# Performance work log

Hardware: AMD Instinct MI355X
Metric: run time of the kernel (lower is better)

Reference implementation:

```python
import jax, jax.numpy as jnp
import numpy as np
from jax import lax

# Module hyperparameters (init_kwargs)
B, T, F, H = 512, 256, 64, 128
D = F + H            # decoder LSTMCell width = input_dim + hidden_rnn
OUT_DIM = 32         # output_dim (survival horizon steps)
RISKS = 2
NEG = -1e10


def lstm_cell(x, h, c, Wih, Whh):
    # PyTorch gate order: i, f, g, o; bias=False
    g = x @ Wih.T + h @ Whh.T
    i, f, gg, o = jnp.split(g, 4, axis=-1)
    c = jax.nn.sigmoid(f) * c + jax.nn.sigmoid(i) * jnp.tanh(gg)
    h = jax.nn.sigmoid(o) * jnp.tanh(c)
    return h, c


def setup_inputs() -> dict:
    key = jax.random.key(0)
    ks = jax.random.split(key, 12)
    rn = lambda k, shp, fan: jax.random.normal(k, shp, jnp.float32) * (1.0 / np.sqrt(fan))
    return {
        "x": jax.random.normal(ks[0], (B, T, F), jnp.float32),
        # encoder LSTM (1 layer, bias=False)
        "W_ih_emb": rn(ks[1], (4 * H, F), F),
        "W_hh_emb": rn(ks[2], (4 * H, H), H),
        # longitudinal head: Linear(H -> F)
        "W_long": rn(ks[3], (F, H), H),
        "b_long": jnp.zeros((F,), jnp.float32),
        # attention head: Linear(F+H -> 1)
        "W_att": rn(ks[4], (1, D), D),
        "b_att": jnp.zeros((1,), jnp.float32),
        # per-risk cause-specific LSTMCell (bias=False) and Linear(D -> 1)
        "W_ih_cs": rn(ks[5], (RISKS, 4 * D, D), D),
        "W_hh_cs": rn(ks[6], (RISKS, 4 * D, D), D),
        "W_cs": rn(ks[7], (RISKS, 1, D), D),
        "b_cs": jnp.zeros((RISKS, 1), jnp.float32),
    }


def _forward(x, W_ih_emb, W_hh_emb, W_long, b_long, W_att, b_att,
             W_ih_cs, W_hh_cs, W_cs, b_cs):
    inputmask = jnp.abs(x).sum(2) == 0                      # [B,T]
    last_obs = (~inputmask).sum(axis=1) - 1                 # [B]

    # encoder LSTM over time
    def enc_step(carry, xt):
        h, c = carry
        h, c = lstm_cell(xt, h, c, W_ih_emb, W_hh_emb)
        return (h, c), h

    h0 = jnp.zeros((x.shape[0], H), x.dtype)
    _, hs = lax.scan(enc_step, (h0, h0), x.transpose(1, 0, 2))
    hidden = hs.transpose(1, 0, 2)                          # [B,T,H]

    long_pred = hidden @ W_long.T + b_long                  # [B,T,F]

    x_last = x[jnp.arange(x.shape[0]), last_obs]            # [B,F]
    concat = jnp.concatenate(
        [hidden, jnp.broadcast_to(x_last[:, None, :], (x.shape[0], x.shape[1], F))], -1)
    scores = (concat @ W_att.T + b_att)[..., 0]             # [B,T]

    idx = jnp.arange(x.shape[1])[None, :]
    scores = jnp.where(idx >= last_obs[:, None], NEG, scores)
    att = jax.nn.softmax(scores, axis=1)
    att = jnp.where((last_obs > 0)[:, None], att, 0.0)      # rows with last_obs==0 zeroed

    hidden_att = jnp.einsum('bt,bth->bh', att, hidden)      # [B,H]
    ha = jnp.concatenate([hidden_att, x_last], 1)           # [B,D]

    state0 = (lax.stop_gradient(ha), lax.stop_gradient(ha))  # .detach() on init state
    rs = jnp.arange(OUT_DIM * RISKS) % RISKS                # k-major, r-minor loop order

    def dec_step(carry, r):
        h, c = carry
        h, c = lstm_cell(ha, h, c, W_ih_cs[r], W_hh_cs[r])
        out = jax.nn.sigmoid(h @ W_cs[r].T + b_cs[r])       # [B,1]
        return (h, c), out

    _, outs = lax.scan(dec_step, state0, rs)                # [steps,B,1]
    outcomes = jax.nn.softmax(outs[..., 0].T, axis=-1)      # [B, OUT_DIM*RISKS]
    parts = tuple(outcomes[:, i * OUT_DIM:(i + 1) * OUT_DIM] for i in range(RISKS))
    return (long_pred,) + parts


def reference(x, W_ih_emb, W_hh_emb, W_long, b_long, W_att, b_att,
              W_ih_cs, W_hh_cs, W_cs, b_cs):
    return _forward(x, W_ih_emb, W_hh_emb, W_long, b_long, W_att, b_att,
                    W_ih_cs, W_hh_cs, W_cs, b_cs)
```

## Files before the change

### kernel.cpp

```cpp
#include <hip/hip_runtime.h>
#include <stdint.h>

#define DEV __device__ __forceinline__
typedef unsigned short u16; typedef unsigned int u32; typedef unsigned long long u64;
typedef __attribute__((ext_vector_type(8))) short s8v;
typedef __attribute__((ext_vector_type(4))) float f4v;

#define Bb 512
#define Tt 256
#define Ff 64
#define Hh 128
#define Dd 192
#define L2E  1.4426950408889634f
#define L2E2 2.8853900817779268f

DEV u16 f2bf(float f){ u32 u = __builtin_bit_cast(u32, f); u32 r = (u + 0x7fffu + ((u>>16)&1u)) >> 16; return (u16)r; }
DEV float bf2f(u16 h){ u32 u = ((u32)h)<<16; return __builtin_bit_cast(float, u); }
DEV float sigm(float x){ return __builtin_amdgcn_rcpf(1.0f + __expf(-x)); }
DEV float ex2(float x){ float r; asm("v_exp_f32 %0, %1" : "=v"(r) : "v"(x)); return r; }
DEV float sig2n(float y){ return __builtin_amdgcn_rcpf(1.0f + ex2(y)); }
DEV float th2 (float y){ return 1.0f - 2.0f*__builtin_amdgcn_rcpf(1.0f + ex2(y)); }
DEV u32 cvtpk(float lo, float hi){ u32 d; asm("v_cvt_pk_bf16_f32 %0, %1, %2" : "=v"(d) : "v"(lo), "v"(hi)); return d; }

DEV f4v mfma16(s8v a, s8v b, f4v c){ return __builtin_amdgcn_mfma_f32_16x16x32_bf16(a, b, c, 0, 0, 0); }

DEV void barrier_lds(){ asm volatile("s_waitcnt lgkmcnt(0)\n\ts_barrier" ::: "memory"); }

DEV int hxe(int k, int c){ int blk = k>>3; return (blk*16 + (c ^ ((blk&3)<<1)))*8 + (k&7); }

DEV s8v pack8s(const float* p, float sc){
  const float4 a = *(const float4*)p; const float4 b = *(const float4*)(p+4);
  s8v r; r[0]=(short)f2bf(a.x*sc); r[1]=(short)f2bf(a.y*sc); r[2]=(short)f2bf(a.z*sc); r[3]=(short)f2bf(a.w*sc);
  r[4]=(short)f2bf(b.x*sc); r[5]=(short)f2bf(b.y*sc); r[6]=(short)f2bf(b.z*sc); r[7]=(short)f2bf(b.w*sc); return r;
}
DEV s8v pack8(const float* p){ return pack8s(p, 1.0f); }
DEV u32 pk2(float a, float b){ return (u32)f2bf(a) | ((u32)f2bf(b)<<16); }

__global__ __launch_bounds__(64) void prelim_k(const float* __restrict__ x,
    const float* __restrict__ Watt, const float* __restrict__ batt,
    float* __restrict__ xlast, float* __restrict__ c0, int* __restrict__ lastobs)
{
  int b = blockIdx.x, tid = threadIdx.x;
  int cnt = 0;
  for (int it = 0; it < 4; ++it){
    int t = it*64 + tid;
    const float4* p = (const float4*)(x + ((size_t)b*Tt + t)*Ff);
    float s = 0.0f;
    #pragma unroll
    for (int q = 0; q < 16; ++q){ float4 v = p[q]; s += fabsf(v.x)+fabsf(v.y)+fabsf(v.z)+fabsf(v.w); }
    u64 m = __ballot(s != 0.0f);
    cnt += __popcll(m);
  }
  int last = cnt - 1;
  int li = (last < 0) ? (Tt-1) : last;
  float xl = x[((size_t)b*Tt + li)*Ff + tid];
  xlast[b*Ff + tid] = xl;
  float p = xl * Watt[Hh + tid];
  for (int off = 32; off; off >>= 1) p += __shfl_down(p, off);
  if (tid == 0){ c0[b] = p + batt[0]; lastobs[b] = last; }
}

__global__ __launch_bounds__(256) void prep_wd_k(const float* __restrict__ Whhcs,
    const float* __restrict__ Wihcs, u16* __restrict__ Wd, u16* __restrict__ WdIH)
{
  int idx = blockIdx.x*256 + threadIdx.x;
  int j = idx & 7, lane = (idx>>3)&63;
  int f = idx>>9;
  int kt = f % 6; int mtr = f/6;
  int mt = mtr % 48, r = mtr/48;
  int ut = mt>>2, g = mt&3;
  int row = g*Dd + ut*16 + (lane&15);
  int k = kt*32 + (lane>>4)*8 + j;
  float sc = (g == 2) ? L2E2 : -L2E;
  size_t src = ((size_t)r*768 + row)*Dd + k;
  Wd[idx]   = f2bf(Whhcs[src] * sc);
  WdIH[idx] = f2bf(Wihcs[src] * sc);
}

__global__ __launch_bounds__(64) void xw_k(const u16* __restrict__ WdIH,
    const float* __restrict__ ha, u16* __restrict__ xwg)
{
  int lane = threadIdx.x, l15 = lane&15, l4 = lane>>4;
  int cg = blockIdx.x & 3, rm = blockIdx.x >> 2;
  s8v af[6];
  #pragma unroll
  for (int kt=0;kt<6;++kt) af[kt] = *(const s8v*)(WdIH + (size_t)(rm*6+kt)*512 + lane*8);
  #pragma unroll
  for (int ct=0; ct<8; ++ct){
    int c = cg*128 + ct*16 + l15;
    f4v a = {0,0,0,0};
    #pragma unroll
    for (int kt=0;kt<6;++kt){
      s8v b = pack8(ha + (size_t)c*Dd + kt*32 + l4*8);
      a = mfma16(af[kt], b, a);
    }
    int bg = cg*8 + ct;
    int base = bg*24576 + rm*256 + l15*16 + l4*4;
    *(u32*)&xwg[base]   = pk2(a[0], a[1]);
    *(u32*)&xwg[base+2] = pk2(a[2], a[3]);
  }
}

__global__ __launch_bounds__(512)
__attribute__((amdgpu_waves_per_eu(2,2)))
void enc_k(
    const float* __restrict__ x, const float* __restrict__ Whh, const float* __restrict__ Wih,
    const float* __restrict__ Wlong, const float* __restrict__ blong, const float* __restrict__ Watt,
    const float* __restrict__ xlast, const float* __restrict__ c0v, const int* __restrict__ lastobs,
    float* __restrict__ lp_out, float* __restrict__ ha)
{
  __shared__ __align__(16) u16 hx[2][3072];
  __shared__ float sarr[2][16];
  const int tid = threadIdx.x, wid = tid>>6, lane = tid&63, l15 = lane&15, l4 = lane>>4;
  const int b0 = blockIdx.x*16;
  const int xrow = tid>>5, xc2 = (tid&31)*2;

  s8v wf[4][6];
  #pragma unroll
  for (int mt = 0; mt < 4; ++mt){
    int gate = mt*Hh + wid*16 + l15;
    float sc = (mt == 2) ? L2E2 : -L2E;
    #pragma unroll
    for (int kt = 0; kt < 6; ++kt){
      int k0 = kt*32 + l4*8;
      if (kt < 4) wf[mt][kt] = pack8s(Whh + (size_t)gate*Hh + k0, sc);
      else        wf[mt][kt] = pack8s(Wih + (size_t)gate*Ff + (k0 - Hh), sc);
    }
  }
  s8v wfx[6];
  {
    s8v z = {0,0,0,0,0,0,0,0};
    #pragma unroll
    for (int kt = 0; kt < 6; ++kt) wfx[kt] = z;
    if (wid < 4){
      int f = wid*16 + l15;
      #pragma unroll
      for (int kt = 0; kt < 4; ++kt) wfx[kt] = pack8(Wlong + (size_t)f*Hh + kt*32 + l4*8);
    } else if (wid == 4 && l15 == 0){
      #pragma unroll
      for (int kt = 0; kt < 4; ++kt) wfx[kt] = pack8(Watt + kt*32 + l4*8);
    }
  }
  float bl[4] = {0,0,0,0};
  if (wid < 4){
    #pragma unroll
    for (int j = 0; j < 4; ++j) bl[j] = blong[wid*16 + l4*4 + j];
  }
  const int   lastb = lastobs[b0 + l15];
  const float c0b   = c0v[b0 + l15];

  const int he0 = hxe(wid*16 + l4*4, l15);
  const int xe0 = hxe(Hh + xc2, xrow);
  float* lpb = lp_out + ((size_t)(b0+l15)*Tt)*Ff + wid*16 + l4*4;

  ((u64*)hx[0])[tid] = 0ull;
  {
    float2 xv = *(const float2*)(x + ((size_t)(b0+xrow)*Tt + 0)*Ff + xc2);
    *(u32*)&hx[0][xe0] = cvtpk(xv.x, xv.y);
  }
  float2 xa = *(const float2*)(x + ((size_t)(b0+xrow)*Tt + 1)*Ff + xc2);
  float2 xb;
  __syncthreads();

  float cst[4] = {0,0,0,0}, hp[4] = {0,0,0,0}, hpp[4] = {0,0,0,0};
  float accA[4] = {0,0,0,0}, mrun = -3.0e38f, zrun = 0.0f;

#define ENC_STEP(T_, CURB_, NXTB_, XC_, XN_) { \
    const int t = (T_); \
    s8v bf[6]; \
    _Pragma("unroll") \
    for (int kt = 0; kt < 6; ++kt) \
      bf[kt] = *(const s8v*)&hx[CURB_][((kt*4 + l4)*16 + (l15 ^ (l4<<1)))*8]; \
    { int tp = t + 2; if (tp > Tt-1) tp = Tt-1; \
      XN_ = *(const float2*)(x + ((size_t)(b0+xrow)*Tt + tp)*Ff + xc2); } \
    f4v acc0 = {0,0,0,0}, acc1 = {0,0,0,0}, acc2 = {0,0,0,0}, acc3 = {0,0,0,0}, accx = {0,0,0,0}; \
    _Pragma("unroll") \
    for (int kt = 0; kt < 6; ++kt){ \
      acc0 = mfma16(wf[0][kt], bf[kt], acc0); \
      acc1 = mfma16(wf[1][kt], bf[kt], acc1); \
      acc2 = mfma16(wf[2][kt], bf[kt], acc2); \
      acc3 = mfma16(wf[3][kt], bf[kt], acc3); \
    } \
    if (wid < 5){ \
      _Pragma("unroll") \
      for (int kt = 0; kt < 6; ++kt) accx = mfma16(wfx[kt], bf[kt], accx); \
    } \
    if (wid == 4 && l4 == 0) sarr[NXTB_][l15] = accx[0] + c0b; \
    float hnew[4]; \
    _Pragma("unroll") \
    for (int j = 0; j < 4; ++j){ \
      float si = sig2n(acc0[j]), sf = sig2n(acc1[j]); \
      float tg = th2(acc2[j]),   so = sig2n(acc3[j]); \
      float cn = sf*cst[j] + si*tg; \
      cst[j] = cn; \
      hnew[j] = so * th2(cn * L2E2); \
    } \
    if (t >= 2){ \
      float sv = sarr[CURB_][l15]; \
      if (t-2 < lastb){ \
        float mn = fmaxf(mrun, sv); \
        float sc = __expf(mrun - mn); \
        float e  = __expf(sv - mn); \
        zrun = zrun*sc + e; \
        _Pragma("unroll") \
        for (int j = 0; j < 4; ++j) accA[j] = accA[j]*sc + e*hpp[j]; \
        mrun = mn; \
      } \
    } \
    _Pragma("unroll") \
    for (int j = 0; j < 4; ++j){ hpp[j] = hp[j]; hp[j] = hnew[j]; } \
    { u32 plo = cvtpk(hnew[0], hnew[1]), phi = cvtpk(hnew[2], hnew[3]); \
      *(u64*)&hx[NXTB_][he0] = (u64)plo | ((u64)phi<<32); } \
    if (t < Tt-1) *(u32*)&hx[NXTB_][xe0] = cvtpk(XC_.x, XC_.y); \
    if (wid < 4 && t >= 1){ \
      float4 v; v.x = accx[0]+bl[0]; v.y = accx[1]+bl[1]; v.z = accx[2]+bl[2]; v.w = accx[3]+bl[3]; \
      *(float4*)(lpb + (size_t)(t-1)*Ff) = v; \
    } \
    barrier_lds(); }

  for (int tp2 = 0; tp2 < 128; ++tp2){
    ENC_STEP(2*tp2,   0, 1, xa, xb)
    ENC_STEP(2*tp2+1, 1, 0, xb, xa)
  }
#undef ENC_STEP

  {
    if (254 < lastb){
      float sv = sarr[0][l15];
      float mn = fmaxf(mrun, sv);
      float sc = __expf(mrun - mn);
      float e  = __expf(sv - mn);
      zrun = zrun*sc + e;
      #pragma unroll
      for (int j = 0; j < 4; ++j) accA[j] = accA[j]*sc + e*hpp[j];
      mrun = mn;
    }
    s8v bfE[4];
    #pragma unroll
    for (int kt = 0; kt < 4; ++kt)
      bfE[kt] = *(const s8v*)&hx[0][((kt*4 + l4)*16 + (l15 ^ (l4<<1)))*8];
    if (wid < 4){
      f4v accx = {0,0,0,0};
      #pragma unroll
      for (int kt = 0; kt < 4; ++kt) accx = mfma16(wfx[kt], bfE[kt], accx);
      float4 v; v.x = accx[0]+bl[0]; v.y = accx[1]+bl[1]; v.z = accx[2]+bl[2]; v.w = accx[3]+bl[3];
      *(float4*)(lpb + (size_t)(Tt-1)*Ff) = v;
    }
    float inv = (zrun > 0.0f) ? __builtin_amdgcn_rcpf(zrun) : 0.0f;
    #pragma unroll
    for (int j = 0; j < 4; ++j)
      ha[(size_t)(b0 + l15)*Dd + wid*16 + l4*4 + j] = accA[j]*inv;
    __syncthreads();
    for (int q = tid; q < 16*Ff; q += 512){
      int r2 = q >> 6, f = q & 63;
      ha[(size_t)(b0 + r2)*Dd + Hh + f] = xlast[(b0 + r2)*Ff + f];
    }
  }
}

__global__ __launch_bounds__(256)
__attribute__((amdgpu_waves_per_eu(1,1)))
void dec_k(const float* __restrict__ ha,
    const u16* __restrict__ Wd, const u16* __restrict__ xwg,
    const float* __restrict__ Wcs, const float* __restrict__ bcs, float* __restrict__ outs)
{
  __shared__ __align__(16) u16 hx[2][3072];
  __shared__ __align__(16) u16 w1[48*2*512];
  __shared__ __align__(16) u16 xwl[2*48*256];
  __shared__ float red[2][4][16];
  const int tid = threadIdx.x, wid = tid>>6, lane = tid&63, l15 = lane&15, l4 = lane>>4;
  const int b0 = blockIdx.x*16;

  #pragma unroll
  for (int it = 0; it < 3; ++it){
    int k = it*64 + (tid>>4)*4, c = tid&15;
    float4 v = *(const float4*)(ha + (size_t)(b0+c)*Dd + k);
    int e = hxe(k, c);
    *(u32*)&hx[0][e]   = cvtpk(v.x, v.y);
    *(u32*)&hx[0][e+2] = cvtpk(v.z, v.w);
  }
  {
    const u16* src = xwg + (size_t)blockIdx.x*24576;
    #pragma unroll
    for (int i = 0; i < 12; ++i){
      int off = (i*256 + tid)*8;
      *(s8v*)&xwl[off] = *(const s8v*)(src + off);
    }
  }
  #pragma unroll
  for (int i = 0; i < 24; ++i){
    int off = (i*256 + tid)*8;
    int chunk = off>>9, inner = off&511;
    int mtg = chunk>>1, kt = chunk&1;
    *(s8v*)&w1[off] = *(const s8v*)(Wd + (size_t)((48+mtg)*6+kt)*512 + inner);
  }
  s8v wreg[12][6];
  #pragma unroll
  for (int m = 0; m < 12; ++m)
    #pragma unroll
    for (int kt = 0; kt < 6; ++kt)
      wreg[m][kt] = *(const s8v*)(Wd + (size_t)((wid*12+m)*6+kt)*512 + lane*8);

  float cst[3][4], wcsr0[3][4], wcsr1[3][4];
  #pragma unroll
  for (int ut = 0; ut < 3; ++ut){
    int u0 = (wid*3+ut)*16 + l4*4;
    #pragma unroll
    for (int jj = 0; jj < 4; ++jj){
      cst[ut][jj]   = ha[(size_t)(b0+l15)*Dd + u0 + jj];
      wcsr0[ut][jj] = Wcs[u0 + jj];
      wcsr1[ut][jj] = Wcs[Dd + u0 + jj];
    }
  }
  const float bc0 = bcs[0], bc1 = bcs[1];
  __syncthreads();

  const u16* wsb = Wd + (size_t)(48 + wid*12)*6*512 + lane*8;
  s8v st[4][4];
#define LOADS_UT(ut_) { \
    _Pragma("unroll") for (int g_=0; g_<4; ++g_) \
      _Pragma("unroll") for (int q_=0; q_<4; ++q_) \
        st[g_][q_] = *(const s8v*)(wsb + (size_t)(((ut_)*4+g_)*6 + 2 + q_)*512); }

#define XWINIT(r_, m_, a_) { \
    int xb_ = ((r_)*48 + wid*12 + (m_))*256 + l15*16 + l4*4; \
    u64 q_ = *(const u64*)&xwl[xb_]; \
    u32 qlo_ = (u32)q_, qhi_ = (u32)(q_>>32); \
    a_[0] = __builtin_bit_cast(float, qlo_<<16); \
    a_[1] = __builtin_bit_cast(float, qlo_ & 0xffff0000u); \
    a_[2] = __builtin_bit_cast(float, qhi_<<16); \
    a_[3] = __builtin_bit_cast(float, qhi_ & 0xffff0000u); }

#define CELLS(ut_, wcs_, nxtb_, a0_, a1_, a2_, a3_) { \
    float hn[4]; \
    _Pragma("unroll") for (int j = 0; j < 4; ++j){ \
      float si = sig2n(a0_[j]), sf = sig2n(a1_[j]); \
      float tg = th2(a2_[j]),   so = sig2n(a3_[j]); \
      float cn = sf*cst[ut_][j] + si*tg; \
      cst[ut_][j] = cn; \
      hn[j] = so * th2(cn * L2E2); \
      part += hn[j] * wcs_[ut_][j]; } \
    u32 plo_ = cvtpk(hn[0], hn[1]), phi_ = cvtpk(hn[2], hn[3]); \
    int u0_ = (wid*3+(ut_))*16 + l4*4; \
    int e0_ = (((u0_>>3)*16) + (l15 ^ (((u0_>>3)&3)<<1)))*8 + (u0_&7); \
    *(u64*)&hx[nxtb_][e0_] = (u64)plo_ | ((u64)phi_<<32); }

  for (int sp = 0; sp < 32; ++sp){
    {
      s8v bf[6];
      #pragma unroll
      for (int kt = 0; kt < 6; ++kt)
        bf[kt] = *(const s8v*)&hx[0][((kt*4 + l4)*16 + (l15 ^ (l4<<1)))*8];
      LOADS_UT(0);
      float part = 0.0f;
      #pragma unroll
      for (int ut = 0; ut < 3; ++ut){
        f4v a0,a1,a2,a3;
        XWINIT(0, ut*4+0, a0); XWINIT(0, ut*4+1, a1); XWINIT(0, ut*4+2, a2); XWINIT(0, ut*4+3, a3);
        #pragma unroll
        for (int kt = 0; kt < 6; ++kt){
          a0 = mfma16(wreg[ut*4+0][kt], bf[kt], a0);
          a1 = mfma16(wreg[ut*4+1][kt], bf[kt], a1);
          a2 = mfma16(wreg[ut*4+2][kt], bf[kt], a2);
          a3 = mfma16(wreg[ut*4+3][kt], bf[kt], a3);
        }
        CELLS(ut, wcsr0, 1, a0, a1, a2, a3);
      }
      part += __shfl_xor(part, 16); part += __shfl_xor(part, 32);
      if (l4 == 0) red[0][wid][l15] = part;
      barrier_lds();
      if (tid < 16)
        outs[(sp*2)*Bb + b0 + tid] = sigm(red[0][0][tid]+red[0][1][tid]+red[0][2][tid]+red[0][3][tid] + bc0);
    }
    {
      s8v bf[6];
      #pragma unroll
      for (int kt = 0; kt < 6; ++kt)
        bf[kt] = *(const s8v*)&hx[1][((kt*4 + l4)*16 + (l15 ^ (l4<<1)))*8];
      float part = 0.0f;
      #pragma unroll
      for (int ut = 0; ut < 3; ++ut){
        f4v a0,a1,a2,a3;
        XWINIT(1, ut*4+0, a0); XWINIT(1, ut*4+1, a1); XWINIT(1, ut*4+2, a2); XWINIT(1, ut*4+3, a3);
        #pragma unroll
        for (int kt = 0; kt < 2; ++kt){
          s8v q0 = *(const s8v*)&w1[((wid*12+ut*4+0)*2+kt)*512 + lane*8];
          s8v q1 = *(const s8v*)&w1[((wid*12+ut*4+1)*2+kt)*512 + lane*8];
          s8v q2 = *(const s8v*)&w1[((wid*12+ut*4+2)*2+kt)*512 + lane*8];
          s8v q3 = *(const s8v*)&w1[((wid*12+ut*4+3)*2+kt)*512 + lane*8];
          a0 = mfma16(q0, bf[kt], a0);
          a1 = mfma16(q1, bf[kt], a1);
          a2 = mfma16(q2, bf[kt], a2);
          a3 = mfma16(q3, bf[kt], a3);
        }
        #pragma unroll
        for (int q = 0; q < 4; ++q){
          a0 = mfma16(st[0][q], bf[2+q], a0);
          a1 = mfma16(st[1][q], bf[2+q], a1);
          a2 = mfma16(st[2][q], bf[2+q], a2);
          a3 = mfma16(st[3][q], bf[2+q], a3);
        }
        if (ut < 2) LOADS_UT(ut+1);
        CELLS(ut, wcsr1, 0, a0, a1, a2, a3);
      }
      part += __shfl_xor(part, 16); part += __shfl_xor(part, 32);
      if (l4 == 0) red[1][wid][l15] = part;
      barrier_lds();
      if (tid < 16)
        outs[(sp*2+1)*Bb + b0 + tid] = sigm(red[1][0][tid]+red[1][1][tid]+red[1][2][tid]+red[1][3][tid] + bc1);
    }
  }
#undef LOADS_UT
#undef XWINIT
#undef CELLS
}

__global__ __launch_bounds__(256) void fin_k(const float* __restrict__ outs, float* __restrict__ dout)
{
  int row = blockIdx.x*256 + threadIdx.x;
  float v[64]; float mx = -3.0e38f;
  #pragma unroll
  for (int s = 0; s < 64; ++s){ v[s] = outs[s*Bb + row]; mx = fmaxf(mx, v[s]); }
  float sum = 0.0f;
  #pragma unroll
  for (int s = 0; s < 64; ++s){ v[s] = __expf(v[s] - mx); sum += v[s]; }
  float inv = __builtin_amdgcn_rcpf(sum);
  float* p0 = dout + (size_t)Bb*Tt*Ff;
  float* p1 = p0 + Bb*32;
  #pragma unroll
  for (int j = 0; j < 32; ++j) p0[row*32 + j] = v[j]*inv;
  #pragma unroll
  for (int j = 0; j < 32; ++j) p1[row*32 + j] = v[32 + j]*inv;
}

extern "C" void kernel_launch(void* const* d_in, const int* in_sizes, int n_in,
                              void* d_out, int out_size, void* d_ws, size_t ws_size,
                              hipStream_t stream)
{
  const float* x      = (const float*)d_in[0];
  const float* Wih    = (const float*)d_in[1];
  const float* Whh    = (const float*)d_in[2];
  const float* Wlong  = (const float*)d_in[3];
  const float* blong  = (const float*)d_in[4];
  const float* Watt   = (const float*)d_in[5];
  const float* batt   = (const float*)d_in[6];
  const float* Wihcs  = (const float*)d_in[7];
  const float* Whhcs  = (const float*)d_in[8];
  const float* Wcs    = (const float*)d_in[9];
  const float* bcs    = (const float*)d_in[10];
  float* out = (float*)d_out;
  char* ws = (char*)d_ws;

  float* xlast   = (float*)ws;
  float* c0      = (float*)(ws + 131072);
  int*   lastobs = (int*)  (ws + 133120);
  float* ha      = (float*)(ws + 135168);
  u16*   Wd      = (u16*)  (ws + 528384);
  u16*   WdIH    = (u16*)  (ws + 1118208);
  u16*   xwg     = (u16*)  (ws + 1708032);
  float* outs    = (float*)(ws + 3280896);

  prep_wd_k<<<1152, 256, 0, stream>>>(Whhcs, Wihcs, Wd, WdIH);
  prelim_k<<<Bb, 64, 0, stream>>>(x, Watt, batt, xlast, c0, lastobs);
  enc_k<<<32, 512, 0, stream>>>(x, Whh, Wih, Wlong, blong, Watt, xlast, c0, lastobs, out, ha);
  xw_k<<<384, 64, 0, stream>>>(WdIH, ha, xwg);
  dec_k<<<32, 256, 0, stream>>>(ha, Wd, xwg, Wcs, bcs, outs);
  fin_k<<<2, 256, 0, stream>>>(outs, out);
}
```

Baseline: 544.1 us.

## Spread decoder across 12 waves with register-resident weights and unswizzled LDS layout

```diff
diff --git a/kernel.cpp b/kernel.cpp
--- a/kernel.cpp
+++ b/kernel.cpp
@@ -15,18 +15,19 @@
 #define L2E2 2.8853900817779268f
 
 DEV u16 f2bf(float f){ u32 u = __builtin_bit_cast(u32, f); u32 r = (u + 0x7fffu + ((u>>16)&1u)) >> 16; return (u16)r; }
-DEV float bf2f(u16 h){ u32 u = ((u32)h)<<16; return __builtin_bit_cast(float, u); }
 DEV float sigm(float x){ return __builtin_amdgcn_rcpf(1.0f + __expf(-x)); }
 DEV float ex2(float x){ float r; asm("v_exp_f32 %0, %1" : "=v"(r) : "v"(x)); return r; }
 DEV float sig2n(float y){ return __builtin_amdgcn_rcpf(1.0f + ex2(y)); }
 DEV float th2 (float y){ return 1.0f - 2.0f*__builtin_amdgcn_rcpf(1.0f + ex2(y)); }
 DEV u32 cvtpk(float lo, float hi){ u32 d; asm("v_cvt_pk_bf16_f32 %0, %1, %2" : "=v"(d) : "v"(lo), "v"(hi)); return d; }
+DEV float blo(u32 q){ return __builtin_bit_cast(float, q<<16); }
+DEV float bhi(u32 q){ return __builtin_bit_cast(float, q & 0xffff0000u); }
 
 DEV f4v mfma16(s8v a, s8v b, f4v c){ return __builtin_amdgcn_mfma_f32_16x16x32_bf16(a, b, c, 0, 0, 0); }
 
 DEV void barrier_lds(){ asm volatile("s_waitcnt lgkmcnt(0)\n\ts_barrier" ::: "memory"); }
 
-DEV int hxe(int k, int c){ int blk = k>>3; return (blk*16 + (c ^ ((blk&3)<<1)))*8 + (k&7); }
+DEV int hxe2(int k, int c){ return (k>>5)*512 + (((k>>3)&3)*16 + c)*8 + (k&7); }
 
 DEV s8v pack8s(const float* p, float sc){
   const float4 a = *(const float4*)p; const float4 b = *(const float4*)(p+4);
@@ -57,7 +58,7 @@
   xlast[b*Ff + tid] = xl;
   float p = xl * Watt[Hh + tid];
   for (int off = 32; off; off >>= 1) p += __shfl_down(p, off);
-  if (tid == 0){ c0[b] = p + batt[0]; lastobs[b] = last; }
+  if (tid == 0){ c0[b] = (p + batt[0]) * L2E; lastobs[b] = last; }
 }
 
 __global__ __launch_bounds__(256) void prep_wd_k(const float* __restrict__ Whhcs,
@@ -138,7 +139,7 @@
       for (int kt = 0; kt < 4; ++kt) wfx[kt] = pack8(Wlong + (size_t)f*Hh + kt*32 + l4*8);
     } else if (wid == 4 && l15 == 0){
       #pragma unroll
-      for (int kt = 0; kt < 4; ++kt) wfx[kt] = pack8(Watt + kt*32 + l4*8);
+      for (int kt = 0; kt < 4; ++kt) wfx[kt] = pack8s(Watt + kt*32 + l4*8, L2E);
     }
   }
   float bl[4] = {0,0,0,0};
@@ -149,8 +150,8 @@
   const int   lastb = lastobs[b0 + l15];
   const float c0b   = c0v[b0 + l15];
 
-  const int he0 = hxe(wid*16 + l4*4, l15);
-  const int xe0 = hxe(Hh + xc2, xrow);
+  const int he0 = hxe2(wid*16 + l4*4, l15);
+  const int xe0 = hxe2(Hh + xc2, xrow);
   float* lpb = lp_out + ((size_t)(b0+l15)*Tt)*Ff + wid*16 + l4*4;
 
   ((u64*)hx[0])[tid] = 0ull;
@@ -170,7 +171,7 @@
     s8v bf[6]; \
     _Pragma("unroll") \
     for (int kt = 0; kt < 6; ++kt) \
-      bf[kt] = *(const s8v*)&hx[CURB_][((kt*4 + l4)*16 + (l15 ^ (l4<<1)))*8]; \
+      bf[kt] = *(const s8v*)&hx[CURB_][kt*512 + lane*8]; \
     { int tp = t + 2; if (tp > Tt-1) tp = Tt-1; \
       XN_ = *(const float2*)(x + ((size_t)(b0+xrow)*Tt + tp)*Ff + xc2); } \
     f4v acc0 = {0,0,0,0}, acc1 = {0,0,0,0}, acc2 = {0,0,0,0}, acc3 = {0,0,0,0}, accx = {0,0,0,0}; \
@@ -199,8 +200,8 @@
       float sv = sarr[CURB_][l15]; \
       if (t-2 < lastb){ \
         float mn = fmaxf(mrun, sv); \
-        float sc = __expf(mrun - mn); \
-        float e  = __expf(sv - mn); \
+        float sc = ex2(mrun - mn); \
+        float e  = ex2(sv - mn); \
         zrun = zrun*sc + e; \
         _Pragma("unroll") \
         for (int j = 0; j < 4; ++j) accA[j] = accA[j]*sc + e*hpp[j]; \
@@ -228,8 +229,8 @@
     if (254 < lastb){
       float sv = sarr[0][l15];
       float mn = fmaxf(mrun, sv);
-      float sc = __expf(mrun - mn);
-      float e  = __expf(sv - mn);
+      float sc = ex2(mrun - mn);
+      float e  = ex2(sv - mn);
       zrun = zrun*sc + e;
       #pragma unroll
       for (int j = 0; j < 4; ++j) accA[j] = accA[j]*sc + e*hpp[j];
@@ -238,7 +239,7 @@
     s8v bfE[4];
     #pragma unroll
     for (int kt = 0; kt < 4; ++kt)
-      bfE[kt] = *(const s8v*)&hx[0][((kt*4 + l4)*16 + (l15 ^ (l4<<1)))*8];
+      bfE[kt] = *(const s8v*)&hx[0][kt*512 + lane*8];
     if (wid < 4){
       f4v accx = {0,0,0,0};
       #pragma unroll
@@ -258,161 +259,93 @@
   }
 }
 
-__global__ __launch_bounds__(256)
-__attribute__((amdgpu_waves_per_eu(1,1)))
+__global__ __launch_bounds__(768)
 void dec_k(const float* __restrict__ ha,
     const u16* __restrict__ Wd, const u16* __restrict__ xwg,
     const float* __restrict__ Wcs, const float* __restrict__ bcs, float* __restrict__ outs)
 {
   __shared__ __align__(16) u16 hx[2][3072];
-  __shared__ __align__(16) u16 w1[48*2*512];
-  __shared__ __align__(16) u16 xwl[2*48*256];
-  __shared__ float red[2][4][16];
+  __shared__ float red[2][12][16];
   const int tid = threadIdx.x, wid = tid>>6, lane = tid&63, l15 = lane&15, l4 = lane>>4;
   const int b0 = blockIdx.x*16;
 
-  #pragma unroll
-  for (int it = 0; it < 3; ++it){
-    int k = it*64 + (tid>>4)*4, c = tid&15;
+  {
+    int k = (tid>>4)*4, c = tid&15;
     float4 v = *(const float4*)(ha + (size_t)(b0+c)*Dd + k);
-    int e = hxe(k, c);
+    int e = hxe2(k, c);
     *(u32*)&hx[0][e]   = cvtpk(v.x, v.y);
     *(u32*)&hx[0][e+2] = cvtpk(v.z, v.w);
   }
-  {
-    const u16* src = xwg + (size_t)blockIdx.x*24576;
-    #pragma unroll
-    for (int i = 0; i < 12; ++i){
-      int off = (i*256 + tid)*8;
-      *(s8v*)&xwl[off] = *(const s8v*)(src + off);
-    }
-  }
-  #pragma unroll
-  for (int i = 0; i < 24; ++i){
-    int off = (i*256 + tid)*8;
-    int chunk = off>>9, inner = off&511;
-    int mtg = chunk>>1, kt = chunk&1;
-    *(s8v*)&w1[off] = *(const s8v*)(Wd + (size_t)((48+mtg)*6+kt)*512 + inner);
-  }
-  s8v wreg[12][6];
-  #pragma unroll
-  for (int m = 0; m < 12; ++m)
-    #pragma unroll
-    for (int kt = 0; kt < 6; ++kt)
-      wreg[m][kt] = *(const s8v*)(Wd + (size_t)((wid*12+m)*6+kt)*512 + lane*8);
-
-  float cst[3][4], wcsr0[3][4], wcsr1[3][4];
-  #pragma unroll
-  for (int ut = 0; ut < 3; ++ut){
-    int u0 = (wid*3+ut)*16 + l4*4;
-    #pragma unroll
-    for (int jj = 0; jj < 4; ++jj){
-      cst[ut][jj]   = ha[(size_t)(b0+l15)*Dd + u0 + jj];
-      wcsr0[ut][jj] = Wcs[u0 + jj];
-      wcsr1[ut][jj] = Wcs[Dd + u0 + jj];
-    }
-  }
-  const float bc0 = bcs[0], bc1 = bcs[1];
-  __syncthreads();
-
-  const u16* wsb = Wd + (size_t)(48 + wid*12)*6*512 + lane*8;
-  s8v st[4][4];
-#define LOADS_UT(ut_) { \
-    _Pragma("unroll") for (int g_=0; g_<4; ++g_) \
-      _Pragma("unroll") for (int q_=0; q_<4; ++q_) \
-        st[g_][q_] = *(const s8v*)(wsb + (size_t)(((ut_)*4+g_)*6 + 2 + q_)*512); }
-
-#define XWINIT(r_, m_, a_) { \
-    int xb_ = ((r_)*48 + wid*12 + (m_))*256 + l15*16 + l4*4; \
-    u64 q_ = *(const u64*)&xwl[xb_]; \
-    u32 qlo_ = (u32)q_, qhi_ = (u32)(q_>>32); \
-    a_[0] = __builtin_bit_cast(float, qlo_<<16); \
-    a_[1] = __builtin_bit_cast(float, qlo_ & 0xffff0000u); \
-    a_[2] = __builtin_bit_cast(float, qhi_<<16); \
-    a_[3] = __builtin_bit_cast(float, qhi_ & 0xffff0000u); }
-
-#define CELLS(ut_, wcs_, nxtb_, a0_, a1_, a2_, a3_) { \
-    float hn[4]; \
-    _Pragma("unroll") for (int j = 0; j < 4; ++j){ \
-      float si = sig2n(a0_[j]), sf = sig2n(a1_[j]); \
-      float tg = th2(a2_[j]),   so = sig2n(a3_[j]); \
-      float cn = sf*cst[ut_][j] + si*tg; \
-      cst[ut_][j] = cn; \
-      hn[j] = so * th2(cn * L2E2); \
-      part += hn[j] * wcs_[ut_][j]; } \
-    u32 plo_ = cvtpk(hn[0], hn[1]), phi_ = cvtpk(hn[2], hn[3]); \
-    int u0_ = (wid*3+(ut_))*16 + l4*4; \
-    int e0_ = (((u0_>>3)*16) + (l15 ^ (((u0_>>3)&3)<<1)))*8 + (u0_&7); \
-    *(u64*)&hx[nxtb_][e0_] = (u64)plo_ | ((u64)phi_<<32); }
-
-  for (int sp = 0; sp < 32; ++sp){
-    {
-      s8v bf[6];
+  s8v wreg[2][4][6];
+  #pragma unroll
+  for (int r = 0; r < 2; ++r)
+    #pragma unroll
+    for (int g = 0; g < 4; ++g)
       #pragma unroll
       for (int kt = 0; kt < 6; ++kt)
-        bf[kt] = *(const s8v*)&hx[0][((kt*4 + l4)*16 + (l15 ^ (l4<<1)))*8];
-      LOADS_UT(0);
-      float part = 0.0f;
-      #pragma unroll
-      for (int ut = 0; ut < 3; ++ut){
-        f4v a0,a1,a2,a3;
-        XWINIT(0, ut*4+0, a0); XWINIT(0, ut*4+1, a1); XWINIT(0, ut*4+2, a2); XWINIT(0, ut*4+3, a3);
-        #pragma unroll
-        for (int kt = 0; kt < 6; ++kt){
-          a0 = mfma16(wreg[ut*4+0][kt], bf[kt], a0);
-          a1 = mfma16(wreg[ut*4+1][kt], bf[kt], a1);
-          a2 = mfma16(wreg[ut*4+2][kt], bf[kt], a2);
-          a3 = mfma16(wreg[ut*4+3][kt], bf[kt], a3);
-        }
-        CELLS(ut, wcsr0, 1, a0, a1, a2, a3);
-      }
-      part += __shfl_xor(part, 16); part += __shfl_xor(part, 32);
-      if (l4 == 0) red[0][wid][l15] = part;
-      barrier_lds();
-      if (tid < 16)
-        outs[(sp*2)*Bb + b0 + tid] = sigm(red[0][0][tid]+red[0][1][tid]+red[0][2][tid]+red[0][3][tid] + bc0);
-    }
-    {
-      s8v bf[6];
-      #pragma unroll
-      for (int kt = 0; kt < 6; ++kt)
-        bf[kt] = *(const s8v*)&hx[1][((kt*4 + l4)*16 + (l15 ^ (l4<<1)))*8];
-      float part = 0.0f;
-      #pragma unroll
-      for (int ut = 0; ut < 3; ++ut){
-        f4v a0,a1,a2,a3;
-        XWINIT(1, ut*4+0, a0); XWINIT(1, ut*4+1, a1); XWINIT(1, ut*4+2, a2); XWINIT(1, ut*4+3, a3);
-        #pragma unroll
-        for (int kt = 0; kt < 2; ++kt){
-          s8v q0 = *(const s8v*)&w1[((wid*12+ut*4+0)*2+kt)*512 + lane*8];
-          s8v q1 = *(const s8v*)&w1[((wid*12+ut*4+1)*2+kt)*512 + lane*8];
-          s8v q2 = *(const s8v*)&w1[((wid*12+ut*4+2)*2+kt)*512 + lane*8];
-          s8v q3 = *(const s8v*)&w1[((wid*12+ut*4+3)*2+kt)*512 + lane*8];
-          a0 = mfma16(q0, bf[kt], a0);
-          a1 = mfma16(q1, bf[kt], a1);
-          a2 = mfma16(q2, bf[kt], a2);
-          a3 = mfma16(q3, bf[kt], a3);
-        }
-        #pragma unroll
-        for (int q = 0; q < 4; ++q){
-          a0 = mfma16(st[0][q], bf[2+q], a0);
-          a1 = mfma16(st[1][q], bf[2+q], a1);
-          a2 = mfma16(st[2][q], bf[2+q], a2);
-          a3 = mfma16(st[3][q], bf[2+q], a3);
-        }
-        if (ut < 2) LOADS_UT(ut+1);
-        CELLS(ut, wcsr1, 0, a0, a1, a2, a3);
-      }
-      part += __shfl_xor(part, 16); part += __shfl_xor(part, 32);
-      if (l4 == 0) red[1][wid][l15] = part;
-      barrier_lds();
-      if (tid < 16)
-        outs[(sp*2+1)*Bb + b0 + tid] = sigm(red[1][0][tid]+red[1][1][tid]+red[1][2][tid]+red[1][3][tid] + bc1);
-    }
-  }
-#undef LOADS_UT
-#undef XWINIT
-#undef CELLS
+        wreg[r][g][kt] = *(const s8v*)(Wd + (size_t)(((r*48 + wid*4 + g)*6) + kt)*512 + lane*8);
+  u32 xwr[2][4][2];
+  #pragma unroll
+  for (int r = 0; r < 2; ++r)
+    #pragma unroll
+    for (int g = 0; g < 4; ++g){
+      int base = blockIdx.x*24576 + (r*48 + wid*4 + g)*256 + l15*16 + l4*4;
+      u64 q = *(const u64*)&xwg[base];
+      xwr[r][g][0] = (u32)q; xwr[r][g][1] = (u32)(q>>32);
+    }
+  const int u0 = wid*16 + l4*4;
+  float cst[4], wcs0[4], wcs1[4];
+  #pragma unroll
+  for (int j = 0; j < 4; ++j){
+    cst[j]  = ha[(size_t)(b0+l15)*Dd + u0 + j];
+    wcs0[j] = Wcs[u0 + j];
+    wcs1[j] = Wcs[Dd + u0 + j];
+  }
+  const float bc0 = bcs[0], bc1 = bcs[1];
+  const int he0 = hxe2(u0, l15);
+  __syncthreads();
+
+#define DEC_STEP(R_, CURB_, NXTB_, WCS_, BC_, S_) { \
+    s8v bf[6]; \
+    _Pragma("unroll") \
+    for (int kt = 0; kt < 6; ++kt) bf[kt] = *(const s8v*)&hx[CURB_][kt*512 + lane*8]; \
+    f4v a0, a1, a2, a3; \
+    { u32 lo, hi; \
+      lo = xwr[R_][0][0]; hi = xwr[R_][0][1]; a0[0]=blo(lo); a0[1]=bhi(lo); a0[2]=blo(hi); a0[3]=bhi(hi); \
+      lo = xwr[R_][1][0]; hi = xwr[R_][1][1]; a1[0]=blo(lo); a1[1]=bhi(lo); a1[2]=blo(hi); a1[3]=bhi(hi); \
+      lo = xwr[R_][2][0]; hi = xwr[R_][2][1]; a2[0]=blo(lo); a2[1]=bhi(lo); a2[2]=blo(hi); a2[3]=bhi(hi); \
+      lo = xwr[R_][3][0]; hi = xwr[R_][3][1]; a3[0]=blo(lo); a3[1]=bhi(lo); a3[2]=blo(hi); a3[3]=bhi(hi); } \
+    _Pragma("unroll") \
+    for (int kt = 0; kt < 6; ++kt){ \
+      a0 = mfma16(wreg[R_][0][kt], bf[kt], a0); \
+      a1 = mfma16(wreg[R_][1][kt], bf[kt], a1); \
+      a2 = mfma16(wreg[R_][2][kt], bf[kt], a2); \
+      a3 = mfma16(wreg[R_][3][kt], bf[kt], a3); } \
+    float part = 0.0f, hn[4]; \
+    _Pragma("unroll") \
+    for (int j = 0; j < 4; ++j){ \
+      float si = sig2n(a0[j]), sf = sig2n(a1[j]); \
+      float tg = th2(a2[j]),   so = sig2n(a3[j]); \
+      float cn = sf*cst[j] + si*tg; \
+      cst[j] = cn; \
+      hn[j] = so * th2(cn * L2E2); \
+      part += hn[j] * WCS_[j]; } \
+    { u32 plo = cvtpk(hn[0], hn[1]), phi = cvtpk(hn[2], hn[3]); \
+      *(u64*)&hx[NXTB_][he0] = (u64)plo | ((u64)phi<<32); } \
+    part += __shfl_xor(part, 16); part += __shfl_xor(part, 32); \
+    if (l4 == 0) red[(S_)&1][wid][l15] = part; \
+    barrier_lds(); \
+    if (tid < 16){ \
+      float ss = BC_; \
+      _Pragma("unroll") \
+      for (int q = 0; q < 12; ++q) ss += red[(S_)&1][q][tid]; \
+      outs[(S_)*Bb + b0 + tid] = sigm(ss); } }
+
+  for (int sp = 0; sp < 32; ++sp){
+    DEC_STEP(0, 0, 1, wcs0, bc0, sp*2)
+    DEC_STEP(1, 1, 0, wcs1, bc1, sp*2+1)
+  }
+#undef DEC_STEP
 }
 
 __global__ __launch_bounds__(256) void fin_k(const float* __restrict__ outs, float* __restrict__ dout)
@@ -464,6 +397,6 @@
   prelim_k<<<Bb, 64, 0, stream>>>(x, Watt, batt, xlast, c0, lastobs);
   enc_k<<<32, 512, 0, stream>>>(x, Whh, Wih, Wlong, blong, Watt, xlast, c0, lastobs, out, ha);
   xw_k<<<384, 64, 0, stream>>>(WdIH, ha, xwg);
-  dec_k<<<32, 256, 0, stream>>>(ha, Wd, xwg, Wcs, bcs, outs);
+  dec_k<<<32, 768, 0, stream>>>(ha, Wd, xwg, Wcs, bcs, outs);
   fin_k<<<2, 256, 0, stream>>>(outs, out);
 }
```

New measurement: 645.4 us. +18.6%, slower.
